# Performance work log

Hardware: AMD Instinct MI355X
Metric: run time of the kernel (lower is better)

## Reference

```python
import jax, jax.numpy as jnp
import numpy as np

N, E, F, H, C, B = 50000, 800000, 256, 256, 10, 64
BN_EPS = 1e-5
ATT_SLOPE = 0.2   # GATConv attention LeakyReLU
ACT_SLOPE = 0.01  # torch.nn.LeakyReLU default

def _leaky(x, slope):
    return jnp.where(x >= 0, x, slope * x)

def _gat_conv(x, src, dst, W, a_src, a_dst, b, n):
    # x:[N,Fin] -> h:[N,Fout]; single-head GATConv with self-loops already in (src,dst)
    h = x @ W
    e_src = h @ a_src  # [N]
    e_dst = h @ a_dst  # [N]
    e = _leaky(e_src[src] + e_dst[dst], ATT_SLOPE)  # [E]
    m = jax.ops.segment_max(e, dst, num_segments=n)
    ex = jnp.exp(e - m[dst])
    s = jax.ops.segment_sum(ex, dst, num_segments=n)
    alpha = ex / s[dst]
    out = jax.ops.segment_sum(alpha[:, None] * h[src], dst, num_segments=n)
    return out + b

def setup_inputs() -> dict:
    key = jax.random.key(0)
    ks = jax.random.split(key, 16)
    x = jax.random.normal(ks[0], (N, F), dtype=jnp.float32)
    edge_index = jax.random.randint(ks[1], (2, E), 0, N, dtype=jnp.int64)
    batch = jnp.sort(jax.random.randint(ks[2], (N,), 0, B, dtype=jnp.int64))
    sc = 0.05
    return {
        "x": x, "edge_index": edge_index, "batch": batch, "batch_size": B,
        "W1": jax.random.normal(ks[3], (F, H), jnp.float32) * sc,
        "a_src1": jax.random.normal(ks[4], (H,), jnp.float32) * sc,
        "a_dst1": jax.random.normal(ks[5], (H,), jnp.float32) * sc,
        "b1": jnp.zeros((H,), jnp.float32),
        "gamma": jnp.ones((H,), jnp.float32),
        "beta": jnp.zeros((H,), jnp.float32),
        "W2": jax.random.normal(ks[6], (H, H), jnp.float32) * sc,
        "a_src2": jax.random.normal(ks[7], (H,), jnp.float32) * sc,
        "a_dst2": jax.random.normal(ks[8], (H,), jnp.float32) * sc,
        "b2": jnp.zeros((H,), jnp.float32),
        "lw1": jax.random.normal(ks[9], (H, H), jnp.float32) * sc,
        "lb1": jnp.zeros((H,), jnp.float32),
        "lw2": jax.random.normal(ks[10], (H, C), jnp.float32) * sc,
        "lb2": jnp.zeros((C,), jnp.float32),
    }

def reference(x, edge_index, batch, batch_size, W1, a_src1, a_dst1, b1,
              gamma, beta, W2, a_src2, a_dst2, b2, lw1, lb1, lw2, lb2):
    n = x.shape[0]
    loops = jnp.arange(n, dtype=edge_index.dtype)
    src = jnp.concatenate([edge_index[0], loops])
    dst = jnp.concatenate([edge_index[1], loops])
    # conv1 + LeakyReLU + BatchNorm (batch statistics, biased var)
    h = _gat_conv(x, src, dst, W1, a_src1, a_dst1, b1, n)
    h = _leaky(h, ACT_SLOPE)
    mean = jnp.mean(h, axis=0)
    var = jnp.var(h, axis=0)
    h = (h - mean) * jax.lax.rsqrt(var + BN_EPS) * gamma + beta
    # conv2 + LeakyReLU
    h = _gat_conv(h, src, dst, W2, a_src2, a_dst2, b2, n)
    h = _leaky(h, ACT_SLOPE)
    # global mean pool over graphs
    sums = jax.ops.segment_sum(h, batch, num_segments=batch_size)
    cnt = jax.ops.segment_sum(jnp.ones((n,), h.dtype), batch, num_segments=batch_size)
    g = sums / jnp.maximum(cnt, 1.0)[:, None]
    # MLP head
    g = _leaky(g @ lw1 + lb1, ACT_SLOPE)
    return g @ lw2 + lb2
```

## Files before the change

### kernel.cpp

```cpp
#include <hip/hip_runtime.h>
#include <math.h>

#define N_NODES 50000
#define N_EDGES 800000
#define ETOT    (N_EDGES + N_NODES)
#define FDIM    256
#define HDIM    256
#define NGRAPH  64
#define C_OUT   10
#define BN_EPS  1e-5f
#define ATT_SLOPE 0.2f
#define ACT_SLOPE 0.01f

#define NBUCK   ((N_NODES + 15) / 16)
#define BCAP    512
#define SORT_NB 192
#define EPB     ((ETOT + SORT_NB - 1) / SORT_NB)

typedef __attribute__((ext_vector_type(8))) short bf16x8;
typedef __attribute__((ext_vector_type(4))) float f32x4;

__device__ __forceinline__ float leaky(float x, float s) { return x >= 0.f ? x : s * x; }

__device__ __forceinline__ float bf2f(unsigned short u) {
    return __uint_as_float((unsigned)u << 16);
}
__device__ __forceinline__ unsigned short f2bf(float f) {
    unsigned u = __float_as_uint(f);
    u += 0x7FFF + ((u >> 16) & 1);
    return (unsigned short)(u >> 16);
}
__device__ __forceinline__ float rlF(float a, int j) {
    return __uint_as_float(__builtin_amdgcn_readlane(__float_as_uint(a), j));
}

__device__ __forceinline__ void gload_lds16(const unsigned short* g, unsigned short* l) {
    __builtin_amdgcn_global_load_lds((const __attribute__((address_space(1))) void*)(g),
                                     (__attribute__((address_space(3))) void*)(l), 16, 0, 0);
}

__device__ __forceinline__ void edge_sd(const int* __restrict__ ei, int e, int& s, int& d) {
    if (e < N_EDGES) { s = ei[e]; d = ei[N_EDGES + e]; }
    else             { s = e - N_EDGES; d = s; }
}

__global__ __launch_bounds__(256) void prep_w(const float* __restrict__ W1,
                                              const float* __restrict__ W2,
                                              unsigned short* __restrict__ Wt1,
                                              unsigned short* __restrict__ Wt2) {
    int wb = blockIdx.x;
    const float* W = (wb < 256) ? W1 : W2;
    unsigned short* Wt = (wb < 256) ? Wt1 : Wt2;
    int idx = (wb & 255) * 256 + threadIdx.x;
    int n = idx >> 8, k = idx & 255;
    Wt[idx] = f2bf(W[k * 256 + n]);
}

__global__ __launch_bounds__(256) void fold_bn(const float* __restrict__ W2,
                                               const float* __restrict__ scale,
                                               const float* __restrict__ shift,
                                               unsigned short* __restrict__ Wt2f,
                                               float* __restrict__ cbias) {
    __shared__ float red[256];
    int n = blockIdx.x, k = threadIdx.x;
    float w = W2[k * 256 + n];
    Wt2f[n * 256 + k] = f2bf(w * scale[k]);
    red[k] = w * shift[k];
    __syncthreads();
    #pragma unroll
    for (int off = 128; off; off >>= 1) {
        if (k < off) red[k] += red[k + off];
        __syncthreads();
    }
    if (k == 0) cbias[n] = red[0];
}

template<bool FROMF32>
__global__ __launch_bounds__(512) void gemm_bf16(const void* __restrict__ Avp,
                                                 const unsigned short* __restrict__ Bt,
                                                 const float* __restrict__ cbias,
                                                 const float* __restrict__ avs,
                                                 const float* __restrict__ avd,
                                                 float* __restrict__ es,
                                                 float* __restrict__ ed,
                                                 unsigned short* __restrict__ C, int M) {
    __shared__ unsigned short Al[128 * 64];
    __shared__ unsigned short Bl[256 * 64];
    __shared__ float lred[4][128][2];
    const int tid = threadIdx.x;
    const int lane = tid & 63;
    const int wid = tid >> 6;
    const int wm = wid >> 2, wn = wid & 3;
    const int row0 = blockIdx.x * 128;
    const int g = lane >> 4, rl = lane & 15;

    f32x4 acc[4][4];
    #pragma unroll
    for (int m = 0; m < 4; ++m)
        #pragma unroll
        for (int n = 0; n < 4; ++n)
            acc[m][n] = (f32x4){0.f, 0.f, 0.f, 0.f};

    for (int kk = 0; kk < 256; kk += 64) {
        if (FROMF32) {
            const float* Af = (const float*)Avp;
            #pragma unroll
            for (int j = 0; j < 2; ++j) {
                int idx = j * 512 + tid;
                int row = idx >> 3, chunk = idx & 7;
                int sc = chunk ^ (row & 7);
                int grow = row0 + row; if (grow >= M) grow = M - 1;
                float4 f0 = *(const float4*)&Af[(size_t)grow * 256 + kk + chunk * 8];
                float4 f1 = *(const float4*)&Af[(size_t)grow * 256 + kk + chunk * 8 + 4];
                uint4 av;
                unsigned short* p = (unsigned short*)&av;
                p[0] = f2bf(f0.x); p[1] = f2bf(f0.y); p[2] = f2bf(f0.z); p[3] = f2bf(f0.w);
                p[4] = f2bf(f1.x); p[5] = f2bf(f1.y); p[6] = f2bf(f1.z); p[7] = f2bf(f1.w);
                *(uint4*)&Al[row * 64 + sc * 8] = av;
            }
        } else {
            const unsigned short* Ab = (const unsigned short*)Avp;
            #pragma unroll
            for (int j = 0; j < 2; ++j) {
                int rowBase = (j * 8 + wid) * 8;
                int row = rowBase + (lane >> 3);
                int grow = row0 + row; if (grow >= M) grow = M - 1;
                int chunk = (lane & 7) ^ (row & 7);
                gload_lds16(&Ab[(size_t)grow * 256 + kk + chunk * 8], &Al[rowBase * 64]);
            }
        }
        #pragma unroll
        for (int j = 0; j < 4; ++j) {
            int colBase = (j * 8 + wid) * 8;
            int col = colBase + (lane >> 3);
            int chunk = (lane & 7) ^ (col & 7);
            gload_lds16(&Bt[(size_t)col * 256 + kk + chunk * 8], &Bl[colBase * 64]);
        }
        __syncthreads();
        #pragma unroll
        for (int ks = 0; ks < 2; ++ks) {
            bf16x8 af[4], bfr[4];
            int chunk = ks * 4 + g;
            #pragma unroll
            for (int m = 0; m < 4; ++m) {
                int row = wm * 64 + m * 16 + rl;
                int sc = chunk ^ (row & 7);
                af[m] = *(const bf16x8*)&Al[row * 64 + sc * 8];
            }
            #pragma unroll
            for (int n = 0; n < 4; ++n) {
                int col = wn * 64 + n * 16 + rl;
                int sc = chunk ^ (col & 7);
                bfr[n] = *(const bf16x8*)&Bl[col * 64 + sc * 8];
            }
            #pragma unroll
            for (int m = 0; m < 4; ++m)
                #pragma unroll
                for (int n = 0; n < 4; ++n)
                    acc[m][n] = __builtin_amdgcn_mfma_f32_16x16x32_bf16(af[m], bfr[n], acc[m][n], 0, 0, 0);
        }
        __syncthreads();
    }
    if (cbias != nullptr) {
        #pragma unroll
        for (int n = 0; n < 4; ++n) {
            float cb = cbias[wn * 64 + n * 16 + rl];
            #pragma unroll
            for (int m = 0; m < 4; ++m)
                #pragma unroll
                for (int r = 0; r < 4; ++r)
                    acc[m][n][r] += cb;
        }
    }
    #pragma unroll
    for (int m = 0; m < 4; ++m) {
        #pragma unroll
        for (int n = 0; n < 4; ++n) {
            int col = wn * 64 + n * 16 + rl;
            #pragma unroll
            for (int r = 0; r < 4; ++r) {
                int row = row0 + wm * 64 + m * 16 + g * 4 + r;
                if (row < M) C[(size_t)row * 256 + col] = f2bf(acc[m][n][r]);
            }
        }
    }
    float as_[4], ad_[4];
    #pragma unroll
    for (int n = 0; n < 4; ++n) {
        int col = wn * 64 + n * 16 + rl;
        as_[n] = avs[col]; ad_[n] = avd[col];
    }
    #pragma unroll
    for (int m = 0; m < 4; ++m) {
        #pragma unroll
        for (int r = 0; r < 4; ++r) {
            float ps = 0.f, pd = 0.f;
            #pragma unroll
            for (int n = 0; n < 4; ++n) {
                float v = acc[m][n][r];
                ps += v * as_[n]; pd += v * ad_[n];
            }
            #pragma unroll
            for (int off = 1; off < 16; off <<= 1) {
                ps += __shfl_xor(ps, off);
                pd += __shfl_xor(pd, off);
            }
            if (rl == 0) {
                int lr = wm * 64 + m * 16 + g * 4 + r;
                lred[wn][lr][0] = ps;
                lred[wn][lr][1] = pd;
            }
        }
    }
    __syncthreads();
    if (tid < 128) {
        int row = row0 + tid;
        if (row < M) {
            es[row] = (lred[0][tid][0] + lred[1][tid][0]) + (lred[2][tid][0] + lred[3][tid][0]);
            ed[row] = (lred[0][tid][1] + lred[1][tid][1]) + (lred[2][tid][1] + lred[3][tid][1]);
        }
    }
}

__global__ __launch_bounds__(256) void count_k(const int* __restrict__ ei,
                                               int* __restrict__ hist2d) {
    __shared__ int lcnt[NBUCK];
    int t = threadIdx.x, blk = blockIdx.x;
    for (int i = t; i < NBUCK; i += 256) lcnt[i] = 0;
    __syncthreads();
    int e0 = blk * EPB, e1 = min(e0 + EPB, ETOT);
    for (int e = e0 + t; e < e1; e += 256) {
        int d = (e < N_EDGES) ? ei[N_EDGES + e] : (e - N_EDGES);
        atomicAdd(&lcnt[d >> 4], 1);
    }
    __syncthreads();
    int* outp = hist2d + blk * NBUCK;
    for (int i = t; i < NBUCK; i += 256) outp[i] = lcnt[i];
}

__global__ __launch_bounds__(256) void colscan_k(int* __restrict__ hist2d,
                                                 int* __restrict__ bcnt) {
    int col = blockIdx.x * 256 + threadIdx.x;
    if (col >= NBUCK) return;
    int run = 0;
    for (int b = 0; b < SORT_NB; ++b) {
        int idx = b * NBUCK + col;
        int c = hist2d[idx];
        hist2d[idx] = run;
        run += c;
    }
    bcnt[col] = run;
}

__global__ __launch_bounds__(256) void scan_buckets(const int* __restrict__ bcnt,
                                                    int* __restrict__ bbase,
                                                    int* __restrict__ row_ptr) {
    __shared__ int s[256];
    constexpr int PER = (NBUCK + 255) / 256;
    int t = threadIdx.x;
    int loc[PER];
    int sum = 0;
    #pragma unroll
    for (int i = 0; i < PER; ++i) {
        int idx = t * PER + i;
        loc[i] = sum;
        sum += (idx < NBUCK) ? bcnt[idx] : 0;
    }
    s[t] = sum;
    __syncthreads();
    #pragma unroll
    for (int off = 1; off < 256; off <<= 1) {
        int add = (t >= off) ? s[t - off] : 0;
        __syncthreads();
        s[t] += add;
        __syncthreads();
    }
    int base = (t > 0) ? s[t - 1] : 0;
    #pragma unroll
    for (int i = 0; i < PER; ++i) {
        int idx = t * PER + i;
        if (idx < NBUCK) bbase[idx] = base + loc[i];
    }
    if (t == 0) row_ptr[N_NODES] = ETOT;
}

__global__ __launch_bounds__(256) void scatter2_k(const int* __restrict__ ei,
                                                  const int* __restrict__ hist2d,
                                                  int* __restrict__ bstore) {
    __shared__ int lcur[NBUCK];
    __shared__ int lbase[NBUCK];
    int t = threadIdx.x, blk = blockIdx.x;
    const int* boff = hist2d + blk * NBUCK;
    for (int i = t; i < NBUCK; i += 256) { lcur[i] = 0; lbase[i] = boff[i]; }
    __syncthreads();
    int e0 = blk * EPB, e1 = min(e0 + EPB, ETOT);
    for (int e = e0 + t; e < e1; e += 256) {
        int s, d; edge_sd(ei, e, s, d);
        int b = d >> 4;
        int r = atomicAdd(&lcur[b], 1);
        int pos = lbase[b] + r;
        if (pos < BCAP) bstore[(size_t)b * BCAP + pos] = s | ((d & 15) << 16);
    }
}

__global__ __launch_bounds__(256) void place_k(const int* __restrict__ bcnt,
                                               const int* __restrict__ bbase,
                                               const int* __restrict__ bstore,
                                               int* __restrict__ row_ptr,
                                               int* __restrict__ csr_src) {
    __shared__ int h16[16], e16[16], c16[16];
    int b = blockIdx.x, t = threadIdx.x;
    if (t < 16) { h16[t] = 0; c16[t] = 0; }
    __syncthreads();
    int sz = bcnt[b]; if (sz > BCAP) sz = BCAP;
    int base = bbase[b];
    const int* bs = bstore + (size_t)b * BCAP;
    int v0 = -1, v1 = -1;
    if (t < sz)       { v0 = bs[t];       atomicAdd(&h16[v0 >> 16], 1); }
    if (t + 256 < sz) { v1 = bs[t + 256]; atomicAdd(&h16[v1 >> 16], 1); }
    __syncthreads();
    if (t == 0) {
        int run = 0;
        #pragma unroll
        for (int j = 0; j < 16; ++j) { e16[j] = run; run += h16[j]; }
    }
    __syncthreads();
    if (t < 16) {
        int d = b * 16 + t;
        if (d < N_NODES) row_ptr[d] = base + e16[t];
    }
    if (v0 >= 0) {
        int dl = v0 >> 16;
        int pos = base + e16[dl] + atomicAdd(&c16[dl], 1);
        csr_src[pos] = v0 & 0xFFFF;
    }
    if (v1 >= 0) {
        int dl = v1 >> 16;
        int pos = base + e16[dl] + atomicAdd(&c16[dl], 1);
        csr_src[pos] = v1 & 0xFFFF;
    }
}

__device__ __forceinline__ void gather4(const unsigned short* __restrict__ hl,
                                        float a, int src, int lim,
                                        float4& A0, float4& A1, float4& A2, float4& A3) {
    int j = 0;
    for (; j + 3 < lim; j += 4) {
        float w0 = rlF(a, j + 0), w1 = rlF(a, j + 1), w2 = rlF(a, j + 2), w3 = rlF(a, j + 3);
        int s0 = __builtin_amdgcn_readlane(src, j + 0);
        int s1 = __builtin_amdgcn_readlane(src, j + 1);
        int s2 = __builtin_amdgcn_readlane(src, j + 2);
        int s3 = __builtin_amdgcn_readlane(src, j + 3);
        ushort4 v0 = *(const ushort4*)&hl[(size_t)s0 * HDIM];
        ushort4 v1 = *(const ushort4*)&hl[(size_t)s1 * HDIM];
        ushort4 v2 = *(const ushort4*)&hl[(size_t)s2 * HDIM];
        ushort4 v3 = *(const ushort4*)&hl[(size_t)s3 * HDIM];
        A0.x += w0 * bf2f(v0.x); A0.y += w0 * bf2f(v0.y); A0.z += w0 * bf2f(v0.z); A0.w += w0 * bf2f(v0.w);
        A1.x += w1 * bf2f(v1.x); A1.y += w1 * bf2f(v1.y); A1.z += w1 * bf2f(v1.z); A1.w += w1 * bf2f(v1.w);
        A2.x += w2 * bf2f(v2.x); A2.y += w2 * bf2f(v2.y); A2.z += w2 * bf2f(v2.z); A2.w += w2 * bf2f(v2.w);
        A3.x += w3 * bf2f(v3.x); A3.y += w3 * bf2f(v3.y); A3.z += w3 * bf2f(v3.z); A3.w += w3 * bf2f(v3.w);
    }
    for (; j < lim; ++j) {
        float w = rlF(a, j);
        int s = __builtin_amdgcn_readlane(src, j);
        ushort4 v = *(const ushort4*)&hl[(size_t)s * HDIM];
        A0.x += w * bf2f(v.x); A0.y += w * bf2f(v.y); A0.z += w * bf2f(v.z); A0.w += w * bf2f(v.w);
    }
}

__global__ __launch_bounds__(256) void dst_agg(const int* __restrict__ row_ptr,
                                               const int* __restrict__ csr_src,
                                               const float* __restrict__ es,
                                               const float* __restrict__ ed,
                                               const unsigned short* __restrict__ h,
                                               const float* __restrict__ bias,
                                               unsigned short* __restrict__ outb) {
    int d = blockIdx.x * 4 + (threadIdx.x >> 6);
    int lane = threadIdx.x & 63;
    if (d >= N_NODES) return;
    float4 b4 = *(const float4*)&bias[lane * 4];
    int start = row_ptr[d], end = row_ptr[d + 1];
    int deg = end - start;
    float edv = ed[d];
    const unsigned short* hl = h + lane * 4;
    float4 A0 = {0,0,0,0}, A1 = {0,0,0,0}, A2 = {0,0,0,0}, A3 = {0,0,0,0};
    float ssum = 0.f;

    if (deg > 0 && deg <= 64) {
        int src = 0; float v = -INFINITY;
        if (lane < deg) {
            src = csr_src[start + lane];
            v = leaky(es[src] + edv, ATT_SLOPE);
        }
        float m = v;
        #pragma unroll
        for (int off = 32; off; off >>= 1) m = fmaxf(m, __shfl_xor(m, off));
        float a = (lane < deg) ? expf(v - m) : 0.f;
        ssum = a;
        gather4(hl, a, src, deg, A0, A1, A2, A3);
    } else if (deg > 64) {
        float m = -INFINITY;
        for (int base = start; base < end; base += 64) {
            int idx = base + lane;
            if (idx < end) m = fmaxf(m, leaky(es[csr_src[idx]] + edv, ATT_SLOPE));
        }
        #pragma unroll
        for (int off = 32; off; off >>= 1) m = fmaxf(m, __shfl_xor(m, off));
        for (int base = start; base < end; base += 64) {
            int idx = base + lane;
            int src = 0; float a = 0.f;
            if (idx < end) {
                src = csr_src[idx];
                a = expf(leaky(es[src] + edv, ATT_SLOPE) - m);
            }
            ssum += a;
            int lim = end - base; if (lim > 64) lim = 64;
            gather4(hl, a, src, lim, A0, A1, A2, A3);
        }
    } else {
        ssum = 1.f;
    }
    #pragma unroll
    for (int off = 32; off; off >>= 1) ssum += __shfl_xor(ssum, off);
    float inv = (deg > 0) ? (1.f / ssum) : 0.f;
    float4 acc;
    acc.x = (A0.x + A1.x) + (A2.x + A3.x);
    acc.y = (A0.y + A1.y) + (A2.y + A3.y);
    acc.z = (A0.z + A1.z) + (A2.z + A3.z);
    acc.w = (A0.w + A1.w) + (A2.w + A3.w);
    ushort4 o;
    o.x = f2bf(leaky(acc.x * inv + b4.x, ACT_SLOPE));
    o.y = f2bf(leaky(acc.y * inv + b4.y, ACT_SLOPE));
    o.z = f2bf(leaky(acc.z * inv + b4.z, ACT_SLOPE));
    o.w = f2bf(leaky(acc.w * inv + b4.w, ACT_SLOPE));
    *(ushort4*)&outb[(size_t)d * HDIM + lane * 4] = o;
}

__global__ __launch_bounds__(256) void bn_stats_k(const unsigned short* __restrict__ buf,
                                                  float* __restrict__ csum,
                                                  float* __restrict__ csq) {
    int t = threadIdx.x;
    int rows_per = (N_NODES + gridDim.x - 1) / gridDim.x;
    int r0 = blockIdx.x * rows_per;
    int r1 = min(r0 + rows_per, N_NODES);
    float sum = 0.f, sq = 0.f;
    for (int r = r0; r < r1; ++r) {
        float v = bf2f(buf[(size_t)r * HDIM + t]);
        sum += v; sq += v * v;
    }
    atomicAdd(&csum[t], sum);
    atomicAdd(&csq[t], sq);
}

__global__ __launch_bounds__(256) void bn_param(const float* __restrict__ csum,
                                                const float* __restrict__ csq,
                                                const float* __restrict__ gamma,
                                                const float* __restrict__ beta,
                                                float* __restrict__ scale,
                                                float* __restrict__ shift) {
    int t = threadIdx.x;
    float mean = csum[t] / (float)N_NODES;
    float var = csq[t] / (float)N_NODES - mean * mean;
    float sc = gamma[t] * rsqrtf(var + BN_EPS);
    scale[t] = sc;
    shift[t] = beta[t] - mean * sc;
}

__global__ __launch_bounds__(256) void post_pool(const unsigned short* __restrict__ buf,
                                                 const int* __restrict__ batch,
                                                 float* __restrict__ gsum,
                                                 float* __restrict__ gcnt) {
    int t = threadIdx.x;
    int rows_per = (N_NODES + gridDim.x - 1) / gridDim.x;
    int r0 = blockIdx.x * rows_per;
    int r1 = min(r0 + rows_per, N_NODES);
    if (r0 >= r1) return;
    int curb = -1; float acc = 0.f; int cnt = 0;
    for (int r = r0; r < r1; ++r) {
        int bb = batch[r];
        if (bb != curb) {
            if (curb >= 0) {
                atomicAdd(&gsum[(size_t)curb * HDIM + t], acc);
                if (t == 0) atomicAdd(&gcnt[curb], (float)cnt);
            }
            curb = bb; acc = 0.f; cnt = 0;
        }
        acc += bf2f(buf[(size_t)r * HDIM + t]);
        cnt++;
    }
    if (curb >= 0) {
        atomicAdd(&gsum[(size_t)curb * HDIM + t], acc);
        if (t == 0) atomicAdd(&gcnt[curb], (float)cnt);
    }
}

__global__ __launch_bounds__(256) void mlp_head(const float* __restrict__ gsum,
                                                const float* __restrict__ gcnt,
                                                const float* __restrict__ lw1,
                                                const float* __restrict__ lb1,
                                                const float* __restrict__ lw2,
                                                const float* __restrict__ lb2,
                                                float* __restrict__ out) {
    __shared__ float g[HDIM];
    __shared__ float hid[HDIM];
    int b = blockIdx.x, t = threadIdx.x;
    float cnt = fmaxf(gcnt[b], 1.f);
    g[t] = gsum[(size_t)b * HDIM + t] / cnt;
    __syncthreads();
    float acc = lb1[t];
    for (int k = 0; k < HDIM; ++k) acc += g[k] * lw1[(size_t)k * HDIM + t];
    hid[t] = leaky(acc, ACT_SLOPE);
    __syncthreads();
    if (t < C_OUT) {
        float o = lb2[t];
        for (int k = 0; k < HDIM; ++k) o += hid[k] * lw2[(size_t)k * C_OUT + t];
        out[(size_t)b * C_OUT + t] = o;
    }
}

extern "C" void kernel_launch(void* const* d_in, const int* in_sizes, int n_in,
                              void* d_out, int out_size, void* d_ws, size_t ws_size,
                              hipStream_t stream) {
    const float* x      = (const float*)d_in[0];
    const int*   ei     = (const int*)d_in[1];
    const int*   batch  = (const int*)d_in[2];
    const float* W1     = (const float*)d_in[4];
    const float* a_src1 = (const float*)d_in[5];
    const float* a_dst1 = (const float*)d_in[6];
    const float* b1     = (const float*)d_in[7];
    const float* gamma  = (const float*)d_in[8];
    const float* beta   = (const float*)d_in[9];
    const float* W2     = (const float*)d_in[10];
    const float* a_src2 = (const float*)d_in[11];
    const float* a_dst2 = (const float*)d_in[12];
    const float* b2     = (const float*)d_in[13];
    const float* lw1    = (const float*)d_in[14];
    const float* lb1    = (const float*)d_in[15];
    const float* lw2    = (const float*)d_in[16];
    const float* lb2    = (const float*)d_in[17];
    float* out = (float*)d_out;

    const size_t NH = (size_t)N_NODES * HDIM;
    char* ws = (char*)d_ws;
    unsigned short* hbf     = (unsigned short*)ws; ws += NH * 2;
    unsigned short* aggbf   = (unsigned short*)ws; ws += NH * 2;
    unsigned short* Wt1     = (unsigned short*)ws; ws += 65536 * 2;
    unsigned short* Wt2     = (unsigned short*)ws; ws += 65536 * 2;
    unsigned short* Wt2f    = (unsigned short*)ws; ws += 65536 * 2;
    float* es      = (float*)ws; ws += N_NODES * 4;
    float* ed      = (float*)ws; ws += N_NODES * 4;
    float* csum    = (float*)ws; ws += HDIM * 4;
    float* csq     = (float*)ws; ws += HDIM * 4;
    float* scale   = (float*)ws; ws += HDIM * 4;
    float* shift   = (float*)ws; ws += HDIM * 4;
    float* cbias   = (float*)ws; ws += HDIM * 4;
    float* gsum    = (float*)ws; ws += NGRAPH * HDIM * 4;
    float* gcnt    = (float*)ws; ws += NGRAPH * 4;
    int*   row_ptr = (int*)ws;   ws += (N_NODES + 1) * 4;
    int*   bcnt    = (int*)ws;   ws += NBUCK * 4;
    int*   bbase   = (int*)ws;   ws += NBUCK * 4;
    int*   hist2d  = (int*)ws;   ws += (size_t)SORT_NB * NBUCK * 4;
    int*   csr_src = (int*)ws;   ws += (size_t)ETOT * 4;
    int*   bstore  = (int*)ws;   ws += (size_t)NBUCK * BCAP * 4;

    const int wave4_blocks = (N_NODES + 3) / 4;
    const int gemm_blocks = (N_NODES + 127) / 128;

    count_k<<<SORT_NB, 256, 0, stream>>>(ei, hist2d);
    colscan_k<<<(NBUCK + 255) / 256, 256, 0, stream>>>(hist2d, bcnt);
    scan_buckets<<<1, 256, 0, stream>>>(bcnt, bbase, row_ptr);
    scatter2_k<<<SORT_NB, 256, 0, stream>>>(ei, hist2d, bstore);
    place_k<<<NBUCK, 256, 0, stream>>>(bcnt, bbase, bstore, row_ptr, csr_src);

    prep_w<<<512, 256, 0, stream>>>(W1, W2, Wt1, Wt2);

    gemm_bf16<true><<<gemm_blocks, 512, 0, stream>>>(x, Wt1, nullptr,
                                                     a_src1, a_dst1, es, ed, hbf, N_NODES);
    dst_agg<<<wave4_blocks, 256, 0, stream>>>(row_ptr, csr_src, es, ed, hbf, b1, aggbf);

    hipMemsetAsync(csum, 0, HDIM * 8, stream);
    bn_stats_k<<<256, 256, 0, stream>>>(aggbf, csum, csq);
    bn_param<<<1, 256, 0, stream>>>(csum, csq, gamma, beta, scale, shift);
    fold_bn<<<256, 256, 0, stream>>>(W2, scale, shift, Wt2f, cbias);

    gemm_bf16<false><<<gemm_blocks, 512, 0, stream>>>(aggbf, Wt2f, cbias,
                                                      a_src2, a_dst2, es, ed, hbf, N_NODES);
    dst_agg<<<wave4_blocks, 256, 0, stream>>>(row_ptr, csr_src, es, ed, hbf, b2, aggbf);

    hipMemsetAsync(gsum, 0, (size_t)(NGRAPH * HDIM + NGRAPH) * 4, stream);
    post_pool<<<256, 256, 0, stream>>>(aggbf, batch, gsum, gcnt);

    mlp_head<<<NGRAPH, 256, 0, stream>>>(gsum, gcnt, lw1, lb1, lw2, lb2, out);
}
```

Before: 333.3 us.

## Process two destination nodes per wavefront in half-wave split aggregation

The aggregation kernel now assigns two destination nodes to each wavefront. When both have degree at most 32, each half-wave handles one node, using 16-byte row loads of 8 bf16 features per lane, and the per-node softmax reductions run over 32 lanes. Otherwise it falls back to the original full-wave path for each node in turn. This is meant to raise memory-level parallelism and halve the wave count for the typical low-degree nodes (average degree about 17), at the cost of divergence when the two nodes' degrees differ. The unused W2 transpose in prep_w is also dropped.

```diff
diff --git a/kernel.cpp b/kernel.cpp
--- a/kernel.cpp
+++ b/kernel.cpp
@@ -45,15 +45,10 @@
 }
 
 __global__ __launch_bounds__(256) void prep_w(const float* __restrict__ W1,
-                                              const float* __restrict__ W2,
-                                              unsigned short* __restrict__ Wt1,
-                                              unsigned short* __restrict__ Wt2) {
-    int wb = blockIdx.x;
-    const float* W = (wb < 256) ? W1 : W2;
-    unsigned short* Wt = (wb < 256) ? Wt1 : Wt2;
-    int idx = (wb & 255) * 256 + threadIdx.x;
+                                              unsigned short* __restrict__ Wt1) {
+    int idx = blockIdx.x * 256 + threadIdx.x;
     int n = idx >> 8, k = idx & 255;
-    Wt[idx] = f2bf(W[k * 256 + n]);
+    Wt1[idx] = f2bf(W1[k * 256 + n]);
 }
 
 __global__ __launch_bounds__(256) void fold_bn(const float* __restrict__ W2,
@@ -368,16 +363,14 @@
     }
 }
 
-__global__ __launch_bounds__(256) void dst_agg(const int* __restrict__ row_ptr,
-                                               const int* __restrict__ csr_src,
-                                               const float* __restrict__ es,
-                                               const float* __restrict__ ed,
-                                               const unsigned short* __restrict__ h,
-                                               const float* __restrict__ bias,
-                                               unsigned short* __restrict__ outb) {
-    int d = blockIdx.x * 4 + (threadIdx.x >> 6);
-    int lane = threadIdx.x & 63;
-    if (d >= N_NODES) return;
+__device__ void dst_one_fullwave(int d, int lane,
+                                 const int* __restrict__ row_ptr,
+                                 const int* __restrict__ csr_src,
+                                 const float* __restrict__ es,
+                                 const float* __restrict__ ed,
+                                 const unsigned short* __restrict__ h,
+                                 const float* __restrict__ bias,
+                                 unsigned short* __restrict__ outb) {
     float4 b4 = *(const float4*)&bias[lane * 4];
     int start = row_ptr[d], end = row_ptr[d + 1];
     int deg = end - start;
@@ -385,7 +378,6 @@
     const unsigned short* hl = h + lane * 4;
     float4 A0 = {0,0,0,0}, A1 = {0,0,0,0}, A2 = {0,0,0,0}, A3 = {0,0,0,0};
     float ssum = 0.f;
-
     if (deg > 0 && deg <= 64) {
         int src = 0; float v = -INFINITY;
         if (lane < deg) {
@@ -434,6 +426,86 @@
     o.z = f2bf(leaky(acc.z * inv + b4.z, ACT_SLOPE));
     o.w = f2bf(leaky(acc.w * inv + b4.w, ACT_SLOPE));
     *(ushort4*)&outb[(size_t)d * HDIM + lane * 4] = o;
+}
+
+__global__ __launch_bounds__(256) void dst_agg(const int* __restrict__ row_ptr,
+                                               const int* __restrict__ csr_src,
+                                               const float* __restrict__ es,
+                                               const float* __restrict__ ed,
+                                               const unsigned short* __restrict__ h,
+                                               const float* __restrict__ bias,
+                                               unsigned short* __restrict__ outb) {
+    int wid = threadIdx.x >> 6;
+    int lane = threadIdx.x & 63;
+    int d0 = blockIdx.x * 8 + wid * 2;
+    int d1 = d0 + 1;
+    int rp0 = row_ptr[d0], rp1 = row_ptr[d1], rp2 = row_ptr[d1 + 1];
+    int deg0 = rp1 - rp0, deg1 = rp2 - rp1;
+
+    if (deg0 > 0 && deg0 <= 32 && deg1 > 0 && deg1 <= 32) {
+        int half = lane >> 5, hl = lane & 31;
+        int myd    = half ? d1 : d0;
+        int mydeg  = half ? deg1 : deg0;
+        int mystart= half ? rp1 : rp0;
+        float edv = ed[myd];
+        int src = 0; float v = -INFINITY;
+        if (hl < mydeg) {
+            src = csr_src[mystart + hl];
+            v = leaky(es[src] + edv, ATT_SLOPE);
+        }
+        float m = v;
+        #pragma unroll
+        for (int off = 16; off; off >>= 1) m = fmaxf(m, __shfl_xor(m, off));
+        float a = (hl < mydeg) ? expf(v - m) : 0.f;
+        float ssum = a;
+        #pragma unroll
+        for (int off = 16; off; off >>= 1) ssum += __shfl_xor(ssum, off);
+        int iters = max(deg0, deg1);
+        float accv[8] = {0.f, 0.f, 0.f, 0.f, 0.f, 0.f, 0.f, 0.f};
+        const unsigned short* hp = h + hl * 8;
+        int j = 0;
+        for (; j + 1 < iters; j += 2) {
+            float wA = __shfl(a, half * 32 + j);
+            int   sA = __shfl(src, half * 32 + j);
+            float wB = __shfl(a, half * 32 + j + 1);
+            int   sB = __shfl(src, half * 32 + j + 1);
+            bool pA = (j < mydeg), pB = (j + 1 < mydeg);
+            if (pA) {
+                uint4 hv = *(const uint4*)&hp[(size_t)sA * HDIM];
+                const unsigned short* p = (const unsigned short*)&hv;
+                #pragma unroll
+                for (int k = 0; k < 8; ++k) accv[k] += wA * bf2f(p[k]);
+            }
+            if (pB) {
+                uint4 hv = *(const uint4*)&hp[(size_t)sB * HDIM];
+                const unsigned short* p = (const unsigned short*)&hv;
+                #pragma unroll
+                for (int k = 0; k < 8; ++k) accv[k] += wB * bf2f(p[k]);
+            }
+        }
+        if (j < iters) {
+            float wA = __shfl(a, half * 32 + j);
+            int   sA = __shfl(src, half * 32 + j);
+            if (j < mydeg) {
+                uint4 hv = *(const uint4*)&hp[(size_t)sA * HDIM];
+                const unsigned short* p = (const unsigned short*)&hv;
+                #pragma unroll
+                for (int k = 0; k < 8; ++k) accv[k] += wA * bf2f(p[k]);
+            }
+        }
+        float inv = 1.f / ssum;
+        float4 bA = *(const float4*)&bias[hl * 8];
+        float4 bB = *(const float4*)&bias[hl * 8 + 4];
+        float bb[8] = {bA.x, bA.y, bA.z, bA.w, bB.x, bB.y, bB.z, bB.w};
+        unsigned short o[8];
+        #pragma unroll
+        for (int k = 0; k < 8; ++k)
+            o[k] = f2bf(leaky(accv[k] * inv + bb[k], ACT_SLOPE));
+        *(uint4*)&outb[(size_t)myd * HDIM + hl * 8] = *(uint4*)o;
+    } else {
+        dst_one_fullwave(d0, lane, row_ptr, csr_src, es, ed, h, bias, outb);
+        dst_one_fullwave(d1, lane, row_ptr, csr_src, es, ed, h, bias, outb);
+    }
 }
 
 __global__ __launch_bounds__(256) void bn_stats_k(const unsigned short* __restrict__ buf,
@@ -545,7 +617,6 @@
     unsigned short* hbf     = (unsigned short*)ws; ws += NH * 2;
     unsigned short* aggbf   = (unsigned short*)ws; ws += NH * 2;
     unsigned short* Wt1     = (unsigned short*)ws; ws += 65536 * 2;
-    unsigned short* Wt2     = (unsigned short*)ws; ws += 65536 * 2;
     unsigned short* Wt2f    = (unsigned short*)ws; ws += 65536 * 2;
     float* es      = (float*)ws; ws += N_NODES * 4;
     float* ed      = (float*)ws; ws += N_NODES * 4;
@@ -563,7 +634,7 @@
     int*   csr_src = (int*)ws;   ws += (size_t)ETOT * 4;
     int*   bstore  = (int*)ws;   ws += (size_t)NBUCK * BCAP * 4;
 
-    const int wave4_blocks = (N_NODES + 3) / 4;
+    const int agg_blocks = (N_NODES + 7) / 8;
     const int gemm_blocks = (N_NODES + 127) / 128;
 
     count_k<<<SORT_NB, 256, 0, stream>>>(ei, hist2d);
@@ -572,11 +643,11 @@
     scatter2_k<<<SORT_NB, 256, 0, stream>>>(ei, hist2d, bstore);
     place_k<<<NBUCK, 256, 0, stream>>>(bcnt, bbase, bstore, row_ptr, csr_src);
 
-    prep_w<<<512, 256, 0, stream>>>(W1, W2, Wt1, Wt2);
+    prep_w<<<256, 256, 0, stream>>>(W1, Wt1);
 
     gemm_bf16<true><<<gemm_blocks, 512, 0, stream>>>(x, Wt1, nullptr,
                                                      a_src1, a_dst1, es, ed, hbf, N_NODES);
-    dst_agg<<<wave4_blocks, 256, 0, stream>>>(row_ptr, csr_src, es, ed, hbf, b1, aggbf);
+    dst_agg<<<agg_blocks, 256, 0, stream>>>(row_ptr, csr_src, es, ed, hbf, b1, aggbf);
 
     hipMemsetAsync(csum, 0, HDIM * 8, stream);
     bn_stats_k<<<256, 256, 0, stream>>>(aggbf, csum, csq);
@@ -585,7 +656,7 @@
 
     gemm_bf16<false><<<gemm_blocks, 512, 0, stream>>>(aggbf, Wt2f, cbias,
                                                       a_src2, a_dst2, es, ed, hbf, N_NODES);
-    dst_agg<<<wave4_blocks, 256, 0, stream>>>(row_ptr, csr_src, es, ed, hbf, b2, aggbf);
+    dst_agg<<<agg_blocks, 256, 0, stream>>>(row_ptr, csr_src, es, ed, hbf, b2, aggbf);
 
     hipMemsetAsync(gsum, 0, (size_t)(NGRAPH * HDIM + NGRAPH) * 4, stream);
     post_pool<<<256, 256, 0, stream>>>(aggbf, batch, gsum, gcnt);
```

Measured after the change: 341.9 us. 1.03x slower.
